# Optimization experiments

Hardware: AMD Instinct MI355X
Metric: run time of the kernel (lower is better)

The kernel has to match this reference:

```python
import jax, jax.numpy as jnp
import numpy as np

NH, NKV, HD, RANK = 16, 4, 128, 512
DIM = NH * HD
EPS = 1.1920928955078125e-07  # torch float32 eps used by F.rms_norm default


def _rms_norm(x):
    return x * jax.lax.rsqrt(jnp.mean(x * x, axis=-1, keepdims=True) + EPS)


def _rope(x, cos, sin):
    # x: [B,H,T,HD]; cos/sin: [T,HD//2]
    h = x.shape[-1] // 2
    x1, x2 = x[..., :h], x[..., h:]
    return jnp.concatenate((x1 * cos + x2 * sin, -x1 * sin + x2 * cos), axis=-1)


def setup_inputs() -> dict:
    key = jax.random.key(0)
    ks = jax.random.split(key, 7)
    B, T = 2, 2048
    s = DIM ** -0.5
    x = jax.random.normal(ks[0], (B, T, DIM), dtype=jnp.float32)
    Wq = jax.random.normal(ks[1], (DIM, DIM), dtype=jnp.float32) * s
    Wdown = jax.random.normal(ks[2], (RANK, DIM), dtype=jnp.float32) * s
    Wkup = jax.random.normal(ks[3], (NKV * HD, RANK), dtype=jnp.float32) * s
    Wvup = jax.random.normal(ks[4], (NKV * HD, RANK), dtype=jnp.float32) * s
    Wproj = jax.random.normal(ks[5], (DIM, DIM), dtype=jnp.float32) * s
    q_gain = jnp.full((NH,), 1.0, dtype=jnp.float32)
    return {"x": x, "Wq": Wq, "Wdown": Wdown, "Wkup": Wkup, "Wvup": Wvup,
            "Wproj": Wproj, "q_gain": q_gain}


def reference(x, Wq, Wdown, Wkup, Wvup, Wproj, q_gain):
    B, T, _ = x.shape
    # q projection -> [B,NH,T,HD], rms-norm per head dim
    q = (x @ Wq.T).reshape(B, T, NH, HD).transpose(0, 2, 1, 3)
    q = _rms_norm(q)
    # low-rank latent kv
    lat = x @ Wdown.T                                   # [B,T,RANK]
    k = (lat @ Wkup.T).reshape(B, T, NKV, HD).transpose(0, 2, 1, 3)
    v = (lat @ Wvup.T).reshape(B, T, NKV, HD).transpose(0, 2, 1, 3)
    k = _rms_norm(k)
    # rotary embeddings
    inv_freq = 1.0 / (10000.0 ** (jnp.arange(0, HD, 2, dtype=jnp.float32) / HD))
    t = jnp.arange(T, dtype=jnp.float32)
    f = jnp.outer(t, inv_freq)                          # [T,HD//2]
    cos, sin = jnp.cos(f), jnp.sin(f)
    q, k = _rope(q, cos, sin), _rope(k, cos, sin)
    q = q * q_gain[None, :, None, None]
    # GQA repeat_interleave kv heads
    rep = NH // NKV
    k = jnp.repeat(k, rep, axis=1)
    v = jnp.repeat(v, rep, axis=1)
    # causal SDPA
    scores = jnp.einsum('bhqd,bhkd->bhqk', q, k) / np.sqrt(HD).astype(np.float32)
    causal = jnp.tril(jnp.ones((T, T), dtype=bool))
    scores = jnp.where(causal, scores, jnp.finfo(scores.dtype).min)
    attn = jax.nn.softmax(scores, axis=-1)
    y = jnp.einsum('bhqk,bhkd->bhqd', attn, v)          # [B,NH,T,HD]
    y = y.transpose(0, 2, 1, 3).reshape(B, T, NH * HD)
    return y @ Wproj.T
```

## Files before the change

### kernel.cpp

```cpp
#include <hip/hip_runtime.h>
#include <stdint.h>

#define B_    2
#define T_    2048
#define NH_   16
#define NKV_  4
#define HD_   128
#define RANK_ 512
#define DIM_  2048
#define BT_   (B_*T_)
#define EPS_  1.1920928955078125e-07f
#define LOG2E_ 1.4426950408889634f

typedef __bf16 bf16x8 __attribute__((ext_vector_type(8)));
typedef float  f32x4  __attribute__((ext_vector_type(4)));

__device__ inline unsigned short f2bf(float f) {
    unsigned int u = __float_as_uint(f);
    u += 0x7fff + ((u >> 16) & 1);
    return (unsigned short)(u >> 16);
}
__device__ inline float bf2f(unsigned short u) {
    return __uint_as_float(((unsigned int)u) << 16);
}
__device__ inline float fast_exp2(float x) { return __builtin_amdgcn_exp2f(x); }

#define GLOAD_LDS16(gp, lp)                                                        \
    __builtin_amdgcn_global_load_lds(                                              \
        (const __attribute__((address_space(1))) void*)(gp),                       \
        (__attribute__((address_space(3))) void*)(lp), 16, 0, 0)

struct CvtArgs {
    const float* src[6];
    unsigned short* dst[6];
    int start4[6];
};
__global__ __launch_bounds__(256) void cvt_all(CvtArgs a, int total4) {
    int i = blockIdx.x * 256 + threadIdx.x;
    if (i >= total4) return;
    int s = 0;
#pragma unroll
    for (int k = 1; k < 6; k++) s += (i >= a.start4[k]) ? 1 : 0;
    int j = i - a.start4[s];
    float4 v = ((const float4*)a.src[s])[j];
    ushort4 o;
    o.x = f2bf(v.x); o.y = f2bf(v.y); o.z = f2bf(v.z); o.w = f2bf(v.w);
    ((ushort4*)a.dst[s])[j] = o;
}

__device__ inline void store_out(float* p, float v) { *p = v; }
__device__ inline void store_out(unsigned short* p, float v) { *p = f2bf(v); }

template <typename OT>
__global__ __launch_bounds__(256) void gemm_bt(const unsigned short* __restrict__ A,
                                               const unsigned short* __restrict__ W,
                                               OT* __restrict__ C,
                                               int M, int N, int K) {
    __shared__ unsigned short As[128][32];
    __shared__ unsigned short Ws[128][32];
    int tid  = threadIdx.x;
    int lane = tid & 63, wave = tid >> 6;
    int quad = lane >> 4, l16 = lane & 15;
    int wm = (wave >> 1) * 64, wn = (wave & 1) * 64;
    long m0 = (long)blockIdx.y * 128, n0 = (long)blockIdx.x * 128;

    int sr = wave * 32 + (lane >> 2);
    int scl = (lane & 3) * 8;
    const unsigned short* Ag0 = A + (m0 + sr) * K + scl;
    const unsigned short* Ag1 = A + (m0 + sr + 16) * K + scl;
    const unsigned short* Wg0 = W + (n0 + sr) * K + scl;
    const unsigned short* Wg1 = W + (n0 + sr + 16) * K + scl;
    unsigned short* Al0 = &As[wave * 32][0];
    unsigned short* Al1 = &As[wave * 32 + 16][0];
    unsigned short* Wl0 = &Ws[wave * 32][0];
    unsigned short* Wl1 = &Ws[wave * 32 + 16][0];

    f32x4 acc[4][4];
#pragma unroll
    for (int i = 0; i < 4; i++)
#pragma unroll
        for (int j = 0; j < 4; j++) acc[i][j] = (f32x4){0.f, 0.f, 0.f, 0.f};

    for (int k0 = 0; k0 < K; k0 += 32) {
        __syncthreads();
        GLOAD_LDS16(Ag0 + k0, Al0);
        GLOAD_LDS16(Ag1 + k0, Al1);
        GLOAD_LDS16(Wg0 + k0, Wl0);
        GLOAD_LDS16(Wg1 + k0, Wl1);
        __syncthreads();
        bf16x8 af[4], wf[4];
#pragma unroll
        for (int i = 0; i < 4; i++) af[i] = *(const bf16x8*)&As[wm + i * 16 + l16][quad * 8];
#pragma unroll
        for (int j = 0; j < 4; j++) wf[j] = *(const bf16x8*)&Ws[wn + j * 16 + l16][quad * 8];
#pragma unroll
        for (int i = 0; i < 4; i++)
#pragma unroll
            for (int j = 0; j < 4; j++)
                acc[i][j] = __builtin_amdgcn_mfma_f32_16x16x32_bf16(af[i], wf[j], acc[i][j], 0, 0, 0);
    }
#pragma unroll
    for (int i = 0; i < 4; i++)
#pragma unroll
        for (int j = 0; j < 4; j++)
#pragma unroll
            for (int r = 0; r < 4; r++) {
                long row = m0 + wm + i * 16 + quad * 4 + r;
                long col = n0 + wn + j * 16 + l16;
                store_out(&C[row * N + col], acc[i][j][r]);
            }
}

__global__ __launch_bounds__(256) void gemm_split(const unsigned short* __restrict__ A,
                                                  const unsigned short* __restrict__ W,
                                                  unsigned short* __restrict__ C1, int N1,
                                                  unsigned short* __restrict__ C2,
                                                  int M, int N, int K) {
    __shared__ unsigned short As[128][32];
    __shared__ unsigned short Ws[128][32];
    int tid  = threadIdx.x;
    int lane = tid & 63, wave = tid >> 6;
    int quad = lane >> 4, l16 = lane & 15;
    int wm = (wave >> 1) * 64, wn = (wave & 1) * 64;
    long m0 = (long)blockIdx.y * 128, n0 = (long)blockIdx.x * 128;

    int sr = wave * 32 + (lane >> 2);
    int scl = (lane & 3) * 8;
    const unsigned short* Ag0 = A + (m0 + sr) * K + scl;
    const unsigned short* Ag1 = A + (m0 + sr + 16) * K + scl;
    const unsigned short* Wg0 = W + (n0 + sr) * K + scl;
    const unsigned short* Wg1 = W + (n0 + sr + 16) * K + scl;
    unsigned short* Al0 = &As[wave * 32][0];
    unsigned short* Al1 = &As[wave * 32 + 16][0];
    unsigned short* Wl0 = &Ws[wave * 32][0];
    unsigned short* Wl1 = &Ws[wave * 32 + 16][0];

    f32x4 acc[4][4];
#pragma unroll
    for (int i = 0; i < 4; i++)
#pragma unroll
        for (int j = 0; j < 4; j++) acc[i][j] = (f32x4){0.f, 0.f, 0.f, 0.f};

    for (int k0 = 0; k0 < K; k0 += 32) {
        __syncthreads();
        GLOAD_LDS16(Ag0 + k0, Al0);
        GLOAD_LDS16(Ag1 + k0, Al1);
        GLOAD_LDS16(Wg0 + k0, Wl0);
        GLOAD_LDS16(Wg1 + k0, Wl1);
        __syncthreads();
        bf16x8 af[4], wf[4];
#pragma unroll
        for (int i = 0; i < 4; i++) af[i] = *(const bf16x8*)&As[wm + i * 16 + l16][quad * 8];
#pragma unroll
        for (int j = 0; j < 4; j++) wf[j] = *(const bf16x8*)&Ws[wn + j * 16 + l16][quad * 8];
#pragma unroll
        for (int i = 0; i < 4; i++)
#pragma unroll
            for (int j = 0; j < 4; j++)
                acc[i][j] = __builtin_amdgcn_mfma_f32_16x16x32_bf16(af[i], wf[j], acc[i][j], 0, 0, 0);
    }
    unsigned short* Cb;
    long ldc, nb;
    if (n0 < N1) { Cb = C1; ldc = N1;     nb = n0; }
    else         { Cb = C2; ldc = N - N1; nb = n0 - N1; }
#pragma unroll
    for (int i = 0; i < 4; i++)
#pragma unroll
        for (int j = 0; j < 4; j++)
#pragma unroll
            for (int r = 0; r < 4; r++) {
                long row = m0 + wm + i * 16 + quad * 4 + r;
                long col = nb + wn + j * 16 + l16;
                Cb[row * ldc + col] = f2bf(acc[i][j][r]);
            }
}

template <int NHEADS, bool GAIN>
__global__ __launch_bounds__(256) void qk_prep(const unsigned short* __restrict__ lin,
                                               const float* __restrict__ gain,
                                               unsigned short* __restrict__ out,
                                               int incols) {
    int r    = blockIdx.x * 4 + (threadIdx.x >> 6);
    int lane = threadIdx.x & 63;
    int bt = r / NHEADS, h = r % NHEADS;
    const unsigned short* ip = lin + (long)bt * incols + h * 128;
    float x1 = bf2f(ip[lane]), x2 = bf2f(ip[lane + 64]);
    float ss = x1 * x1 + x2 * x2;
#pragma unroll
    for (int off = 32; off; off >>= 1) ss += __shfl_xor(ss, off);
    float inv = rsqrtf(ss * (1.0f / 128.0f) + EPS_);
    x1 *= inv; x2 *= inv;
    int b = bt / T_, t = bt % T_;
    float freq = expf(-(float)lane * 0.14391156463f);
    float f = (float)t * freq;
    float s, c;
    sincosf(f, &s, &c);
    float g = GAIN ? gain[h] * 0.08838834764831845f * LOG2E_ : 1.0f;
    float o1 = (x1 * c + x2 * s) * g;
    float o2 = (x2 * c - x1 * s) * g;
    unsigned short* op = out + ((long)(b * NHEADS + h) * T_ + t) * 128;
    op[lane]      = f2bf(o1);
    op[lane + 64] = f2bf(o2);
}

__global__ __launch_bounds__(256) void v_transpose(const unsigned short* __restrict__ vlin,
                                                   unsigned short* __restrict__ vt) {
    __shared__ unsigned short tile[32][33];
    int bkv = blockIdx.z, b = bkv >> 2, kv = bkv & 3;
    int t0 = blockIdx.x * 32, d0 = blockIdx.y * 32;
    int tx = threadIdx.x & 31, ty = threadIdx.x >> 5;
#pragma unroll
    for (int rr = 0; rr < 32; rr += 8) {
        int t = t0 + ty + rr;
        tile[ty + rr][tx] = vlin[((long)(b * T_ + t)) * 1024 + 512 + kv * 128 + d0 + tx];
    }
    __syncthreads();
#pragma unroll
    for (int rr = 0; rr < 32; rr += 8) {
        int d = d0 + ty + rr;
        vt[((long)((b * NKV_ + kv) * 128 + d)) * T_ + t0 + tx] = tile[tx][ty + rr];
    }
}

__global__ __launch_bounds__(256, 3) void attn_kernel(const unsigned short* __restrict__ Q,
                                                      const unsigned short* __restrict__ Km,
                                                      const unsigned short* __restrict__ Vt,
                                                      unsigned short* __restrict__ po,
                                                      float* __restrict__ pm,
                                                      float* __restrict__ pl) {
    __shared__ alignas(16) unsigned short Vs2[2][128][32];
    __shared__ alignas(16) unsigned short KsPt[4 * 32 * 72];

    int tid = threadIdx.x, lane = tid & 63, wave = tid >> 6;
    int quad = lane >> 4, l16 = lane & 15;

    int g8 = blockIdx.x & 7;
    int j5 = blockIdx.x >> 3;
    int hh = j5 / 40;
    int rem = j5 % 40;
    int b = g8 >> 2, kvh = g8 & 3, h = kvh * 4 + hh, bh = b * 16 + h;
    int g, loc;
    if      (rem <  4) { g = 0; loc = rem;      }
    else if (rem < 12) { g = 1; loc = rem - 4;  }
    else if (rem < 24) { g = 2; loc = rem - 12; }
    else               { g = 3; loc = rem - 24; }
    int qb = g * 4 + loc / (g + 1);
    int c  = loc % (g + 1);
    int Q0 = qb * 128 + wave * 32;

    int kt0 = c * 8;
    int nt  = min(8, 2 * qb + 2 - kt0);

    const unsigned short* qp = Q + ((long)(b * NH_ + h) * T_ + Q0) * 128;
    const char* kb = (const char*)(Km + (long)(b * NKV_ + kvh) * T_ * 128);
    const char* vb = (const char*)(Vt + (long)(b * NKV_ + kvh) * 128 * (long)T_);
    char* ksB = (char*)&KsPt[0];
    char* vsB = (char*)&Vs2[0][0][0];
    unsigned short* PtW = &KsPt[wave * 2304];

    bf16x8 Qf[2][4];
#pragma unroll
    for (int u = 0; u < 2; u++)
#pragma unroll
        for (int s = 0; s < 4; s++)
            Qf[u][s] = *(const bf16x8*)&qp[(u * 16 + l16) * 128 + s * 32 + quad * 8];

    f32x4 Ot[8][2];
#pragma unroll
    for (int n = 0; n < 8; n++)
#pragma unroll
        for (int u = 0; u < 2; u++) Ot[n][u] = (f32x4){0.f, 0.f, 0.f, 0.f};
    float mr[2] = {-3.0e38f, -3.0e38f}, ls[2] = {0.f, 0.f};

    for (int kt = kt0; kt < kt0 + nt; kt++) {
        int tb = kt * 64;
        __syncthreads();
        {
            const char* kg = kb + (long)tb * 256 + wave * 64 + (lane >> 2) * 256 + (lane & 3) * 16;
            char* kl = ksB + wave * 4096 + lane * 16;
#pragma unroll
            for (int r = 0; r < 4; r++)
                GLOAD_LDS16(kg + r * 4096, kl + r * 1024);
        }
        {
            int h2 = wave >> 1;
            int D0 = (wave & 1) * 64;
#pragma unroll
            for (int r = 0; r < 4; r++) {
                int D = D0 + r * 16;
                const char* vgr = vb + (long)(D + (lane >> 2)) * 4096 + (long)tb * 2 + h2 * 64 + (lane & 3) * 16;
                char* vl = vsB + h2 * 8192 + D * 64 + lane * 16;
                GLOAD_LDS16(vgr, vl);
            }
        }
        __syncthreads();

        f32x4 sc[4][2];
#pragma unroll
        for (int j = 0; j < 4; j++)
#pragma unroll
            for (int u = 0; u < 2; u++) sc[j][u] = (f32x4){0.f, 0.f, 0.f, 0.f};
#pragma unroll
        for (int j = 0; j < 4; j++)
#pragma unroll
            for (int s = 0; s < 4; s++) {
                bf16x8 kf = *(const bf16x8*)&KsPt[s * 2048 + (j * 16 + l16) * 32 + quad * 8];
                sc[j][0] = __builtin_amdgcn_mfma_f32_16x16x32_bf16(kf, Qf[0][s], sc[j][0], 0, 0, 0);
                sc[j][1] = __builtin_amdgcn_mfma_f32_16x16x32_bf16(kf, Qf[1][s], sc[j][1], 0, 0, 0);
            }
        __syncthreads();

#pragma unroll
        for (int u = 0; u < 2; u++) {
            if (tb + 63 > Q0 + u * 16) {
                int qg = Q0 + u * 16 + l16;
#pragma unroll
                for (int j = 0; j < 4; j++)
#pragma unroll
                    for (int r = 0; r < 4; r++) {
                        int kvg = tb + j * 16 + quad * 4 + r;
                        if (kvg > qg) sc[j][u][r] = -3.0e38f;
                    }
            }
            float mx = -3.0e38f;
#pragma unroll
            for (int j = 0; j < 4; j++)
#pragma unroll
                for (int r = 0; r < 4; r++) mx = fmaxf(mx, sc[j][u][r]);
            mx = fmaxf(mx, __shfl_xor(mx, 16));
            mx = fmaxf(mx, __shfl_xor(mx, 32));
            float mnew  = fmaxf(mr[u], mx);
            float alpha = fast_exp2(mr[u] - mnew);
            float ps = 0.f;
#pragma unroll
            for (int j = 0; j < 4; j++) {
                ushort4 pk;
                float p0 = fast_exp2(sc[j][u][0] - mnew);
                float p1 = fast_exp2(sc[j][u][1] - mnew);
                float p2 = fast_exp2(sc[j][u][2] - mnew);
                float p3 = fast_exp2(sc[j][u][3] - mnew);
                ps += (p0 + p1) + (p2 + p3);
                pk.x = f2bf(p0); pk.y = f2bf(p1); pk.z = f2bf(p2); pk.w = f2bf(p3);
                *(ushort4*)&PtW[(u * 16 + l16) * 72 + j * 16 + quad * 4] = pk;
            }
            ps += __shfl_xor(ps, 16);
            ps += __shfl_xor(ps, 32);
            ls[u] = ls[u] * alpha + ps;
            mr[u] = mnew;
#pragma unroll
            for (int n = 0; n < 8; n++) Ot[n][u] *= alpha;
        }
        __threadfence_block();

#pragma unroll
        for (int h2 = 0; h2 < 2; h2++) {
            bf16x8 pf0 = *(const bf16x8*)&PtW[(0 * 16 + l16) * 72 + h2 * 32 + quad * 8];
            bf16x8 pf1 = *(const bf16x8*)&PtW[(1 * 16 + l16) * 72 + h2 * 32 + quad * 8];
#pragma unroll
            for (int n = 0; n < 8; n++) {
                bf16x8 vf = *(const bf16x8*)&Vs2[h2][n * 16 + l16][quad * 8];
                Ot[n][0] = __builtin_amdgcn_mfma_f32_16x16x32_bf16(vf, pf0, Ot[n][0], 0, 0, 0);
                Ot[n][1] = __builtin_amdgcn_mfma_f32_16x16x32_bf16(vf, pf1, Ot[n][1], 0, 0, 0);
            }
        }
    }

    int i2 = qb * 4 + wave;
    long slot = (long)bh * 160 + 8 * g * (g + 1) + (long)(i2 & 15) * (g + 1) + c;
#pragma unroll
    for (int half = 0; half < 2; half++) {
        __threadfence_block();
#pragma unroll
        for (int n2 = 0; n2 < 4; n2++) {
            int n = half * 4 + n2;
#pragma unroll
            for (int u = 0; u < 2; u++) {
                ushort4 pk;
                pk.x = f2bf(Ot[n][u][0]); pk.y = f2bf(Ot[n][u][1]);
                pk.z = f2bf(Ot[n][u][2]); pk.w = f2bf(Ot[n][u][3]);
                *(ushort4*)&PtW[(u * 16 + l16) * 72 + n2 * 16 + quad * 4] = pk;
            }
        }
        __threadfence_block();
#pragma unroll
        for (int rr = 0; rr < 4; rr++) {
            int qrow = rr * 8 + (lane >> 3);
            int colseg = (lane & 7) * 8;
            uint4 val = *(const uint4*)&PtW[qrow * 72 + colseg];
            *(uint4*)&po[slot * 4096 + qrow * 128 + half * 64 + colseg] = val;
        }
    }
    if (lane < 16) {
        pm[slot * 32 + lane]      = mr[0];
        pm[slot * 32 + 16 + lane] = mr[1];
        pl[slot * 32 + lane]      = ls[0];
        pl[slot * 32 + 16 + lane] = ls[1];
    }
}

__global__ __launch_bounds__(256) void attn_combine(const unsigned short* __restrict__ po,
                                                    const float* __restrict__ pm,
                                                    const float* __restrict__ pl,
                                                    unsigned short* __restrict__ Y) {
    int bh = blockIdx.x >> 6, i2 = blockIdx.x & 63;
    int g = i2 >> 4, nc = g + 1;
    long slot0 = (long)bh * 160 + 8 * g * (g + 1) + (long)(i2 & 15) * nc;
    int col = threadIdx.x & 127;
    int r0  = threadIdx.x >> 7;
    int b = bh >> 4, h = bh & 15;
    for (int r = r0; r < 32; r += 2) {
        float M = -3.0e38f;
        for (int c = 0; c < nc; c++) M = fmaxf(M, pm[(slot0 + c) * 32 + r]);
        float L = 0.f, acc = 0.f;
        for (int c = 0; c < nc; c++) {
            float w = fast_exp2(pm[(slot0 + c) * 32 + r] - M);
            L   += pl[(slot0 + c) * 32 + r] * w;
            acc += w * bf2f(po[(slot0 + c) * 4096 + r * 128 + col]);
        }
        Y[((long)b * T_ + i2 * 32 + r) * DIM_ + h * 128 + col] = f2bf(acc / L);
    }
}

extern "C" void kernel_launch(void* const* d_in, const int* in_sizes, int n_in,
                              void* d_out, int out_size, void* d_ws, size_t ws_size,
                              hipStream_t stream) {
    const float* x     = (const float*)d_in[0];
    const float* Wq    = (const float*)d_in[1];
    const float* Wdown = (const float*)d_in[2];
    const float* Wkup  = (const float*)d_in[3];
    const float* Wvup  = (const float*)d_in[4];
    const float* Wproj = (const float*)d_in[5];
    const float* qgain = (const float*)d_in[6];

    char* ws = (char*)d_ws;
    size_t off = 0;
    auto alloc = [&](size_t bytes) -> void* {
        void* p = ws + off;
        off += (bytes + 255) & ~(size_t)255;
        return p;
    };
    unsigned short* Wp_bf  = (unsigned short*)alloc((size_t)DIM_ * DIM_ * 2);
    unsigned short* q_bf   = (unsigned short*)alloc((size_t)BT_ * DIM_ * 2);
    unsigned short* k_bf   = (unsigned short*)alloc((size_t)B_ * NKV_ * T_ * 128 * 2);
    unsigned short* vT_bf  = (unsigned short*)alloc((size_t)B_ * NKV_ * T_ * 128 * 2);
    unsigned short* y_bf   = (unsigned short*)alloc((size_t)BT_ * DIM_ * 2);
    char* region2 = ws + off;
    unsigned short* x_bf   = (unsigned short*)alloc((size_t)BT_ * DIM_ * 2);
    unsigned short* Wqd_bf = (unsigned short*)alloc((size_t)2560 * DIM_ * 2);
    unsigned short* Wkv_bf = (unsigned short*)alloc((size_t)1024 * RANK_ * 2);
    unsigned short* q_lin  = (unsigned short*)alloc((size_t)BT_ * DIM_ * 2);
    unsigned short* lat_bf = (unsigned short*)alloc((size_t)BT_ * RANK_ * 2);
    unsigned short* kv_lin = (unsigned short*)alloc((size_t)BT_ * 1024 * 2);

    unsigned short* po = (unsigned short*)region2;
    float* pm = (float*)(region2 + (size_t)5120 * 4096 * 2);
    float* pl = pm + 5120 * 32;

    CvtArgs ca;
    ca.src[0] = x;     ca.dst[0] = x_bf;
    ca.src[1] = Wq;    ca.dst[1] = Wqd_bf;
    ca.src[2] = Wdown; ca.dst[2] = Wqd_bf + (size_t)DIM_ * DIM_;
    ca.src[3] = Wkup;  ca.dst[3] = Wkv_bf;
    ca.src[4] = Wvup;  ca.dst[4] = Wkv_bf + (size_t)512 * RANK_;
    ca.src[5] = Wproj; ca.dst[5] = Wp_bf;
    int n4[6] = {BT_ * DIM_ / 4, DIM_ * DIM_ / 4, RANK_ * DIM_ / 4,
                 512 * RANK_ / 4, 512 * RANK_ / 4, DIM_ * DIM_ / 4};
    int acc4 = 0;
    for (int i = 0; i < 6; i++) { ca.start4[i] = acc4; acc4 += n4[i]; }
    cvt_all<<<(acc4 + 255) / 256, 256, 0, stream>>>(ca, acc4);

    gemm_split<<<dim3(2560 / 128, BT_ / 128), 256, 0, stream>>>(x_bf, Wqd_bf, q_lin, DIM_, lat_bf, BT_, 2560, DIM_);
    gemm_bt<unsigned short><<<dim3(1024 / 128, BT_ / 128), 256, 0, stream>>>(lat_bf, Wkv_bf, kv_lin, BT_, 1024, RANK_);

    qk_prep<NH_, true><<<BT_ * NH_ / 4, 256, 0, stream>>>(q_lin, qgain, q_bf, DIM_);
    qk_prep<NKV_, false><<<BT_ * NKV_ / 4, 256, 0, stream>>>(kv_lin, qgain, k_bf, 1024);
    v_transpose<<<dim3(T_ / 32, 128 / 32, B_ * NKV_), 256, 0, stream>>>(kv_lin, vT_bf);

    attn_kernel<<<dim3(32 * 40), 256, 0, stream>>>(q_bf, k_bf, vT_bf, po, pm, pl);
    attn_combine<<<dim3(32 * 64), 256, 0, stream>>>(po, pm, pl, y_bf);

    gemm_bt<float><<<dim3(DIM_ / 128, BT_ / 128), 256, 0, stream>>>(y_bf, Wp_bf, (float*)d_out, BT_, DIM_, DIM_);
}
```

Before: 406.4 us.

## Deepen GEMM K-step, fuse prep kernels, rebalance attention split into smaller chunks

The GEMM kernels now load two 32-wide K slices per barrier pair, halving the number of synchronizations per K. The three q/k prep and v-transpose launches are merged into one kernel to cut launch overhead. The attention work split changes from 8-tile chunks with 40 jobs per group to 6-tile chunks with 51 jobs, issued heaviest-first, for better load balance across CUs. The cost is more partial results for the combine pass to read and merge, and twice the LDS per GEMM block.

After: 398.9 us. About the same (-1.8%).

```diff
diff --git a/kernel.cpp b/kernel.cpp
--- a/kernel.cpp
+++ b/kernel.cpp
@@ -11,6 +11,8 @@
 #define BT_   (B_*T_)
 #define EPS_  1.1920928955078125e-07f
 #define LOG2E_ 1.4426950408889634f
+#define CT_   6
+#define SLOTS_PER_BH_ 204
 
 typedef __bf16 bf16x8 __attribute__((ext_vector_type(8)));
 typedef float  f32x4  __attribute__((ext_vector_type(4)));
@@ -56,8 +58,8 @@
                                                const unsigned short* __restrict__ W,
                                                OT* __restrict__ C,
                                                int M, int N, int K) {
-    __shared__ unsigned short As[128][32];
-    __shared__ unsigned short Ws[128][32];
+    __shared__ unsigned short As[2][128][32];
+    __shared__ unsigned short Ws[2][128][32];
     int tid  = threadIdx.x;
     int lane = tid & 63, wave = tid >> 6;
     int quad = lane >> 4, l16 = lane & 15;
@@ -70,10 +72,10 @@
     const unsigned short* Ag1 = A + (m0 + sr + 16) * K + scl;
     const unsigned short* Wg0 = W + (n0 + sr) * K + scl;
     const unsigned short* Wg1 = W + (n0 + sr + 16) * K + scl;
-    unsigned short* Al0 = &As[wave * 32][0];
-    unsigned short* Al1 = &As[wave * 32 + 16][0];
-    unsigned short* Wl0 = &Ws[wave * 32][0];
-    unsigned short* Wl1 = &Ws[wave * 32 + 16][0];
+    unsigned short* Al0 = &As[0][wave * 32][0];
+    unsigned short* Al1 = &As[0][wave * 32 + 16][0];
+    unsigned short* Wl0 = &Ws[0][wave * 32][0];
+    unsigned short* Wl1 = &Ws[0][wave * 32 + 16][0];
 
     f32x4 acc[4][4];
 #pragma unroll
@@ -81,23 +83,30 @@
 #pragma unroll
         for (int j = 0; j < 4; j++) acc[i][j] = (f32x4){0.f, 0.f, 0.f, 0.f};
 
-    for (int k0 = 0; k0 < K; k0 += 32) {
+    for (int k0 = 0; k0 < K; k0 += 64) {
         __syncthreads();
         GLOAD_LDS16(Ag0 + k0, Al0);
         GLOAD_LDS16(Ag1 + k0, Al1);
         GLOAD_LDS16(Wg0 + k0, Wl0);
         GLOAD_LDS16(Wg1 + k0, Wl1);
-        __syncthreads();
-        bf16x8 af[4], wf[4];
-#pragma unroll
-        for (int i = 0; i < 4; i++) af[i] = *(const bf16x8*)&As[wm + i * 16 + l16][quad * 8];
-#pragma unroll
-        for (int j = 0; j < 4; j++) wf[j] = *(const bf16x8*)&Ws[wn + j * 16 + l16][quad * 8];
-#pragma unroll
-        for (int i = 0; i < 4; i++)
-#pragma unroll
-            for (int j = 0; j < 4; j++)
-                acc[i][j] = __builtin_amdgcn_mfma_f32_16x16x32_bf16(af[i], wf[j], acc[i][j], 0, 0, 0);
+        GLOAD_LDS16(Ag0 + k0 + 32, Al0 + 4096);
+        GLOAD_LDS16(Ag1 + k0 + 32, Al1 + 4096);
+        GLOAD_LDS16(Wg0 + k0 + 32, Wl0 + 4096);
+        GLOAD_LDS16(Wg1 + k0 + 32, Wl1 + 4096);
+        __syncthreads();
+#pragma unroll
+        for (int p = 0; p < 2; p++) {
+            bf16x8 af[4], wf[4];
+#pragma unroll
+            for (int i = 0; i < 4; i++) af[i] = *(const bf16x8*)&As[p][wm + i * 16 + l16][quad * 8];
+#pragma unroll
+            for (int j = 0; j < 4; j++) wf[j] = *(const bf16x8*)&Ws[p][wn + j * 16 + l16][quad * 8];
+#pragma unroll
+            for (int i = 0; i < 4; i++)
+#pragma unroll
+                for (int j = 0; j < 4; j++)
+                    acc[i][j] = __builtin_amdgcn_mfma_f32_16x16x32_bf16(af[i], wf[j], acc[i][j], 0, 0, 0);
+        }
     }
 #pragma unroll
     for (int i = 0; i < 4; i++)
@@ -116,8 +125,8 @@
                                                   unsigned short* __restrict__ C1, int N1,
                                                   unsigned short* __restrict__ C2,
                                                   int M, int N, int K) {
-    __shared__ unsigned short As[128][32];
-    __shared__ unsigned short Ws[128][32];
+    __shared__ unsigned short As[2][128][32];
+    __shared__ unsigned short Ws[2][128][32];
     int tid  = threadIdx.x;
     int lane = tid & 63, wave = tid >> 6;
     int quad = lane >> 4, l16 = lane & 15;
@@ -130,10 +139,10 @@
     const unsigned short* Ag1 = A + (m0 + sr + 16) * K + scl;
     const unsigned short* Wg0 = W + (n0 + sr) * K + scl;
     const unsigned short* Wg1 = W + (n0 + sr + 16) * K + scl;
-    unsigned short* Al0 = &As[wave * 32][0];
-    unsigned short* Al1 = &As[wave * 32 + 16][0];
-    unsigned short* Wl0 = &Ws[wave * 32][0];
-    unsigned short* Wl1 = &Ws[wave * 32 + 16][0];
+    unsigned short* Al0 = &As[0][wave * 32][0];
+    unsigned short* Al1 = &As[0][wave * 32 + 16][0];
+    unsigned short* Wl0 = &Ws[0][wave * 32][0];
+    unsigned short* Wl1 = &Ws[0][wave * 32 + 16][0];
 
     f32x4 acc[4][4];
 #pragma unroll
@@ -141,23 +150,30 @@
 #pragma unroll
         for (int j = 0; j < 4; j++) acc[i][j] = (f32x4){0.f, 0.f, 0.f, 0.f};
 
-    for (int k0 = 0; k0 < K; k0 += 32) {
+    for (int k0 = 0; k0 < K; k0 += 64) {
         __syncthreads();
         GLOAD_LDS16(Ag0 + k0, Al0);
         GLOAD_LDS16(Ag1 + k0, Al1);
         GLOAD_LDS16(Wg0 + k0, Wl0);
         GLOAD_LDS16(Wg1 + k0, Wl1);
-        __syncthreads();
-        bf16x8 af[4], wf[4];
-#pragma unroll
-        for (int i = 0; i < 4; i++) af[i] = *(const bf16x8*)&As[wm + i * 16 + l16][quad * 8];
-#pragma unroll
-        for (int j = 0; j < 4; j++) wf[j] = *(const bf16x8*)&Ws[wn + j * 16 + l16][quad * 8];
-#pragma unroll
-        for (int i = 0; i < 4; i++)
-#pragma unroll
-            for (int j = 0; j < 4; j++)
-                acc[i][j] = __builtin_amdgcn_mfma_f32_16x16x32_bf16(af[i], wf[j], acc[i][j], 0, 0, 0);
+        GLOAD_LDS16(Ag0 + k0 + 32, Al0 + 4096);
+        GLOAD_LDS16(Ag1 + k0 + 32, Al1 + 4096);
+        GLOAD_LDS16(Wg0 + k0 + 32, Wl0 + 4096);
+        GLOAD_LDS16(Wg1 + k0 + 32, Wl1 + 4096);
+        __syncthreads();
+#pragma unroll
+        for (int p = 0; p < 2; p++) {
+            bf16x8 af[4], wf[4];
+#pragma unroll
+            for (int i = 0; i < 4; i++) af[i] = *(const bf16x8*)&As[p][wm + i * 16 + l16][quad * 8];
+#pragma unroll
+            for (int j = 0; j < 4; j++) wf[j] = *(const bf16x8*)&Ws[p][wn + j * 16 + l16][quad * 8];
+#pragma unroll
+            for (int i = 0; i < 4; i++)
+#pragma unroll
+                for (int j = 0; j < 4; j++)
+                    acc[i][j] = __builtin_amdgcn_mfma_f32_16x16x32_bf16(af[i], wf[j], acc[i][j], 0, 0, 0);
+        }
     }
     unsigned short* Cb;
     long ldc, nb;
@@ -175,50 +191,59 @@
             }
 }
 
-template <int NHEADS, bool GAIN>
-__global__ __launch_bounds__(256) void qk_prep(const unsigned short* __restrict__ lin,
-                                               const float* __restrict__ gain,
-                                               unsigned short* __restrict__ out,
-                                               int incols) {
-    int r    = blockIdx.x * 4 + (threadIdx.x >> 6);
-    int lane = threadIdx.x & 63;
-    int bt = r / NHEADS, h = r % NHEADS;
-    const unsigned short* ip = lin + (long)bt * incols + h * 128;
-    float x1 = bf2f(ip[lane]), x2 = bf2f(ip[lane + 64]);
-    float ss = x1 * x1 + x2 * x2;
-#pragma unroll
-    for (int off = 32; off; off >>= 1) ss += __shfl_xor(ss, off);
-    float inv = rsqrtf(ss * (1.0f / 128.0f) + EPS_);
-    x1 *= inv; x2 *= inv;
-    int b = bt / T_, t = bt % T_;
-    float freq = expf(-(float)lane * 0.14391156463f);
-    float f = (float)t * freq;
-    float s, c;
-    sincosf(f, &s, &c);
-    float g = GAIN ? gain[h] * 0.08838834764831845f * LOG2E_ : 1.0f;
-    float o1 = (x1 * c + x2 * s) * g;
-    float o2 = (x2 * c - x1 * s) * g;
-    unsigned short* op = out + ((long)(b * NHEADS + h) * T_ + t) * 128;
-    op[lane]      = f2bf(o1);
-    op[lane + 64] = f2bf(o2);
-}
-
-__global__ __launch_bounds__(256) void v_transpose(const unsigned short* __restrict__ vlin,
-                                                   unsigned short* __restrict__ vt) {
-    __shared__ unsigned short tile[32][33];
-    int bkv = blockIdx.z, b = bkv >> 2, kv = bkv & 3;
-    int t0 = blockIdx.x * 32, d0 = blockIdx.y * 32;
-    int tx = threadIdx.x & 31, ty = threadIdx.x >> 5;
-#pragma unroll
-    for (int rr = 0; rr < 32; rr += 8) {
-        int t = t0 + ty + rr;
-        tile[ty + rr][tx] = vlin[((long)(b * T_ + t)) * 1024 + 512 + kv * 128 + d0 + tx];
-    }
-    __syncthreads();
-#pragma unroll
-    for (int rr = 0; rr < 32; rr += 8) {
-        int d = d0 + ty + rr;
-        vt[((long)((b * NKV_ + kv) * 128 + d)) * T_ + t0 + tx] = tile[tx][ty + rr];
+__global__ __launch_bounds__(256) void prep_all(const unsigned short* __restrict__ q_lin,
+                                                const unsigned short* __restrict__ kv_lin,
+                                                const float* __restrict__ gain,
+                                                unsigned short* __restrict__ q_bf,
+                                                unsigned short* __restrict__ k_bf,
+                                                unsigned short* __restrict__ vt) {
+    int bid = blockIdx.x;
+    if (bid < 20480) {
+        bool isQ = bid < 16384;
+        int nheads = isQ ? NH_ : NKV_;
+        int incols = isQ ? DIM_ : 1024;
+        const unsigned short* lin = isQ ? q_lin : kv_lin;
+        unsigned short* out = isQ ? q_bf : k_bf;
+        int base = isQ ? bid : bid - 16384;
+        int r    = base * 4 + (threadIdx.x >> 6);
+        int lane = threadIdx.x & 63;
+        int bt = r / nheads, h = r % nheads;
+        const unsigned short* ip = lin + (long)bt * incols + h * 128;
+        float x1 = bf2f(ip[lane]), x2 = bf2f(ip[lane + 64]);
+        float ss = x1 * x1 + x2 * x2;
+#pragma unroll
+        for (int off = 32; off; off >>= 1) ss += __shfl_xor(ss, off);
+        float inv = rsqrtf(ss * (1.0f / 128.0f) + EPS_);
+        x1 *= inv; x2 *= inv;
+        int b = bt / T_, t = bt % T_;
+        float freq = expf(-(float)lane * 0.14391156463f);
+        float f = (float)t * freq;
+        float s, c;
+        sincosf(f, &s, &c);
+        float g = isQ ? gain[h] * 0.08838834764831845f * LOG2E_ : 1.0f;
+        float o1 = (x1 * c + x2 * s) * g;
+        float o2 = (x2 * c - x1 * s) * g;
+        unsigned short* op = out + ((long)(b * nheads + h) * T_ + t) * 128;
+        op[lane]      = f2bf(o1);
+        op[lane + 64] = f2bf(o2);
+    } else {
+        __shared__ unsigned short tile[32][33];
+        int idx = bid - 20480;
+        int tt = idx & 63, dd = (idx >> 6) & 3, bkv = idx >> 8;
+        int b = bkv >> 2, kv = bkv & 3;
+        int t0 = tt * 32, d0 = dd * 32;
+        int tx = threadIdx.x & 31, ty = threadIdx.x >> 5;
+#pragma unroll
+        for (int rr = 0; rr < 32; rr += 8) {
+            int t = t0 + ty + rr;
+            tile[ty + rr][tx] = kv_lin[((long)(b * T_ + t)) * 1024 + 512 + kv * 128 + d0 + tx];
+        }
+        __syncthreads();
+#pragma unroll
+        for (int rr = 0; rr < 32; rr += 8) {
+            int d = d0 + ty + rr;
+            vt[((long)((b * NKV_ + kv) * 128 + d)) * T_ + t0 + tx] = tile[tx][ty + rr];
+        }
     }
 }
 
@@ -236,20 +261,19 @@
 
     int g8 = blockIdx.x & 7;
     int j5 = blockIdx.x >> 3;
-    int hh = j5 / 40;
-    int rem = j5 % 40;
+    int hh = j5 / 51;
+    int rem = 50 - (j5 % 51);
     int b = g8 >> 2, kvh = g8 & 3, h = kvh * 4 + hh, bh = b * 16 + h;
-    int g, loc;
-    if      (rem <  4) { g = 0; loc = rem;      }
-    else if (rem < 12) { g = 1; loc = rem - 4;  }
-    else if (rem < 24) { g = 2; loc = rem - 12; }
-    else               { g = 3; loc = rem - 24; }
-    int qb = g * 4 + loc / (g + 1);
-    int c  = loc % (g + 1);
+    int a = 0;
+    while (a < 5 && 3 * (a + 1) * (a + 2) / 2 <= rem) a++;
+    int off = rem - 3 * a * (a + 1) / 2;
+    int nc = a + 1;
+    int qb = (a == 5) ? 15 : (3 * a + off / nc);
+    int c  = (a == 5) ? off : (off % nc);
     int Q0 = qb * 128 + wave * 32;
 
-    int kt0 = c * 8;
-    int nt  = min(8, 2 * qb + 2 - kt0);
+    int kt0 = c * CT_;
+    int nt  = min(CT_, 2 * qb + 2 - kt0);
 
     const unsigned short* qp = Q + ((long)(b * NH_ + h) * T_ + Q0) * 128;
     const char* kb = (const char*)(Km + (long)(b * NKV_ + kvh) * T_ * 128);
@@ -365,8 +389,7 @@
         }
     }
 
-    int i2 = qb * 4 + wave;
-    long slot = (long)bh * 160 + 8 * g * (g + 1) + (long)(i2 & 15) * (g + 1) + c;
+    long slot = (long)bh * SLOTS_PER_BH_ + 4 * (rem - c) + wave * nc + c;
 #pragma unroll
     for (int half = 0; half < 2; half++) {
         __threadfence_block();
@@ -403,8 +426,11 @@
                                                     const float* __restrict__ pl,
                                                     unsigned short* __restrict__ Y) {
     int bh = blockIdx.x >> 6, i2 = blockIdx.x & 63;
-    int g = i2 >> 4, nc = g + 1;
-    long slot0 = (long)bh * 160 + 8 * g * (g + 1) + (long)(i2 & 15) * nc;
+    int qb = i2 >> 2, w = i2 & 3;
+    int a = (qb == 15) ? 5 : qb / 3;
+    int nc = a + 1;
+    int S = 3 * a * (a + 1) / 2 + (qb - 3 * a) * nc;
+    long slot0 = (long)bh * SLOTS_PER_BH_ + 4 * S + w * nc;
     int col = threadIdx.x & 127;
     int r0  = threadIdx.x >> 7;
     int b = bh >> 4, h = bh & 15;
@@ -413,9 +439,9 @@
         for (int c = 0; c < nc; c++) M = fmaxf(M, pm[(slot0 + c) * 32 + r]);
         float L = 0.f, acc = 0.f;
         for (int c = 0; c < nc; c++) {
-            float w = fast_exp2(pm[(slot0 + c) * 32 + r] - M);
-            L   += pl[(slot0 + c) * 32 + r] * w;
-            acc += w * bf2f(po[(slot0 + c) * 4096 + r * 128 + col]);
+            float wgt = fast_exp2(pm[(slot0 + c) * 32 + r] - M);
+            L   += pl[(slot0 + c) * 32 + r] * wgt;
+            acc += wgt * bf2f(po[(slot0 + c) * 4096 + r * 128 + col]);
         }
         Y[((long)b * T_ + i2 * 32 + r) * DIM_ + h * 128 + col] = f2bf(acc / L);
     }
@@ -452,9 +478,10 @@
     unsigned short* lat_bf = (unsigned short*)alloc((size_t)BT_ * RANK_ * 2);
     unsigned short* kv_lin = (unsigned short*)alloc((size_t)BT_ * 1024 * 2);
 
+    const size_t NSLOT = 32 * SLOTS_PER_BH_;
     unsigned short* po = (unsigned short*)region2;
-    float* pm = (float*)(region2 + (size_t)5120 * 4096 * 2);
-    float* pl = pm + 5120 * 32;
+    float* pm = (float*)(region2 + NSLOT * 4096 * 2);
+    float* pl = pm + NSLOT * 32;
 
     CvtArgs ca;
     ca.src[0] = x;     ca.dst[0] = x_bf;
@@ -472,11 +499,9 @@
     gemm_split<<<dim3(2560 / 128, BT_ / 128), 256, 0, stream>>>(x_bf, Wqd_bf, q_lin, DIM_, lat_bf, BT_, 2560, DIM_);
     gemm_bt<unsigned short><<<dim3(1024 / 128, BT_ / 128), 256, 0, stream>>>(lat_bf, Wkv_bf, kv_lin, BT_, 1024, RANK_);
 
-    qk_prep<NH_, true><<<BT_ * NH_ / 4, 256, 0, stream>>>(q_lin, qgain, q_bf, DIM_);
-    qk_prep<NKV_, false><<<BT_ * NKV_ / 4, 256, 0, stream>>>(kv_lin, qgain, k_bf, 1024);
-    v_transpose<<<dim3(T_ / 32, 128 / 32, B_ * NKV_), 256, 0, stream>>>(kv_lin, vT_bf);
-
-    attn_kernel<<<dim3(32 * 40), 256, 0, stream>>>(q_bf, k_bf, vT_bf, po, pm, pl);
+    prep_all<<<16384 + 4096 + 2048, 256, 0, stream>>>(q_lin, kv_lin, qgain, q_bf, k_bf, vT_bf);
+
+    attn_kernel<<<dim3(8 * SLOTS_PER_BH_), 256, 0, stream>>>(q_bf, k_bf, vT_bf, po, pm, pl);
     attn_combine<<<dim3(32 * 64), 256, 0, stream>>>(po, pm, pl, y_bf);
 
     gemm_bt<float><<<dim3(DIM_ / 128, BT_ / 128), 256, 0, stream>>>(y_bf, Wp_bf, (float*)d_out, BT_, DIM_, DIM_);
```
